# Kernel optimization log

Hardware: AMD Instinct MI355X
Metric: run time of the kernel (lower is better)

Reference implementation:

```python
import jax, jax.numpy as jnp
import numpy as np

N_NODES = 50000
N_EDGES = 20000
EDGE_SIZE = 32
IN_CH = 256
OUT_CH = 256


def setup_inputs() -> dict:
    key = jax.random.key(0)
    k1, k2, k3 = jax.random.split(key, 3)
    x = jax.random.normal(k1, (N_NODES, IN_CH), dtype=jnp.float32)
    hyperedges = jax.random.randint(k2, (N_EDGES, EDGE_SIZE), 0, N_NODES)
    weight = jax.random.normal(k3, (IN_CH, OUT_CH), dtype=jnp.float32)
    return {"x": x, "hyperedges": hyperedges, "weight": weight}


def reference(x, hyperedges, weight):
    # Gather node features per hyperedge and reduce ('sum' aggregation):
    # [E, K, C] -> [E, C]
    edge_sum = x[hyperedges].sum(axis=1)
    # Scatter-add each hyperedge's summed feature back to every member node.
    agg = jnp.zeros_like(x).at[hyperedges].add(edge_sum[:, None, :])
    # Dense projection + ReLU.
    return jax.nn.relu(agg @ weight)
```

## Files before the change

kernel.cpp:

```cpp
#include <hip/hip_runtime.h>
#include <hip/hip_bf16.h>
#include <hip/hip_fp16.h>

#define N_NODES 50000
#define N_EDGES 20000
#define EDGE_K  32
#define CH      256
#define N_INC   (N_EDGES * EDGE_K)
#define ELL_CAP 64
#define NSLICE  8
#define SCH     32
#define ZROW    N_EDGES

typedef __attribute__((ext_vector_type(4))) float f32x4;
typedef __attribute__((ext_vector_type(8))) _Float16 f16x8;

static __device__ __forceinline__ __half2 u2h2(unsigned int u) {
    __half2 h; __builtin_memcpy(&h, &u, 4); return h;
}
static __device__ __forceinline__ unsigned int h22u(__half2 h) {
    unsigned int u; __builtin_memcpy(&u, &h, 4); return u;
}
static __device__ __forceinline__ unsigned int pk2h(float a, float b) {
    return h22u(__halves2half2(__float2half_rn(a), __float2half_rn(b)));
}

#define FILL_GROUPS   8
#define NODES_PER_GRP (N_NODES / FILL_GROUPS)
#define FILL_WIN      2560
#define FILL_BLOCKS   ((N_INC / FILL_WIN) * FILL_GROUPS)
#define CONV_BLOCKS   (N_NODES * CH / 8 / 256)
__global__ void prep_kernel(const float* __restrict__ x, unsigned short* __restrict__ xb,
                            const float* __restrict__ w, unsigned short* __restrict__ wt,
                            const int* __restrict__ he, int* __restrict__ deg,
                            unsigned short* __restrict__ ell, unsigned short* __restrict__ yb) {
    int b = blockIdx.x;
    if (b < FILL_BLOCKS) {
        int g  = b % FILL_GROUPS;
        int wn = b / FILL_GROUPS;
        int lo = g * NODES_PER_GRP, hi = lo + NODES_PER_GRP;
        int base = wn * FILL_WIN;
#pragma unroll
        for (int it = 0; it < FILL_WIN / 256; ++it) {
            int i = base + it * 256 + threadIdx.x;
            int node = he[i];
            if (node >= lo && node < hi) {
                int slot = atomicAdd(&deg[node], 1);
                if (slot < ELL_CAP)
                    ell[(size_t)node * ELL_CAP + slot] = (unsigned short)(i >> 5);
            }
        }
    } else if (b < FILL_BLOCKS + CONV_BLOCKS) {
        int i = (b - FILL_BLOCKS) * 256 + threadIdx.x;
        int n = i >> 5, sub = i & 31;
        int g = sub >> 2, cp = (sub & 3) * 8;
        const float* src = x + (size_t)n * CH + sub * 8;
        f32x4 v0 = *reinterpret_cast<const f32x4*>(src);
        f32x4 v1 = *reinterpret_cast<const f32x4*>(src + 4);
        uint4 u;
        u.x = pk2h(v0.x, v0.y);
        u.y = pk2h(v0.z, v0.w);
        u.z = pk2h(v1.x, v1.y);
        u.w = pk2h(v1.z, v1.w);
        *reinterpret_cast<uint4*>(xb + ((size_t)g * N_NODES + n) * SCH + cp) = u;
    } else if (b < FILL_BLOCKS + CONV_BLOCKS + CH) {
        int n = b - FILL_BLOCKS - CONV_BLOCKS;
        int k = threadIdx.x;
        __half h = __float2half_rn(w[k * CH + n]);
        wt[n * CH + k] = *reinterpret_cast<unsigned short*>(&h);
    } else {
        int g = threadIdx.x >> 5, c = threadIdx.x & 31;
        yb[((size_t)g * (N_EDGES + 1) + ZROW) * SCH + c] = 0;
    }
}

#define GGRP          (N_EDGES / 16)
#define GATHER_BLOCKS (GGRP * NSLICE)
__global__ __launch_bounds__(256, 4) void gather_kernel(
        const unsigned short* __restrict__ xb, const int* __restrict__ he,
        unsigned short* __restrict__ es) {
    int gb  = blockIdx.x;
    int g   = gb & 7;
    int grp = gb >> 3;
    int w = threadIdx.x >> 6, lane = threadIdx.x & 63;
    int ebase = grp * 16 + w * 4;
    const int* hp = he + (size_t)ebase * EDGE_K;
    int s = lane & 15;
    int ep = lane >> 4, k = (lane >> 2) & 3, q = lane & 3;
    int mA = hp[ep * 32 + s];
    int mB = hp[ep * 32 + 16 + s];
    const unsigned short* xg = xb + (size_t)g * N_NODES * SCH;
    int hb = lane & 48;
    int e0 = __shfl(mA, hb + ((0 + k) & 15), 64);
    int e1 = __shfl(mA, hb + ((4 + k) & 15), 64);
    int e2 = __shfl(mA, hb + ((8 + k) & 15), 64);
    int e3 = __shfl(mA, hb + ((12 + k) & 15), 64);
    int e4 = __shfl(mB, hb + ((0 + k) & 15), 64);
    int e5 = __shfl(mB, hb + ((4 + k) & 15), 64);
    int e6 = __shfl(mB, hb + ((8 + k) & 15), 64);
    int e7 = __shfl(mB, hb + ((12 + k) & 15), 64);
    uint4 d0 = *reinterpret_cast<const uint4*>(xg + (size_t)e0 * SCH + q * 8);
    uint4 d1 = *reinterpret_cast<const uint4*>(xg + (size_t)e1 * SCH + q * 8);
    uint4 d2 = *reinterpret_cast<const uint4*>(xg + (size_t)e2 * SCH + q * 8);
    uint4 d3 = *reinterpret_cast<const uint4*>(xg + (size_t)e3 * SCH + q * 8);
    uint4 d4 = *reinterpret_cast<const uint4*>(xg + (size_t)e4 * SCH + q * 8);
    uint4 d5 = *reinterpret_cast<const uint4*>(xg + (size_t)e5 * SCH + q * 8);
    uint4 d6 = *reinterpret_cast<const uint4*>(xg + (size_t)e6 * SCH + q * 8);
    uint4 d7 = *reinterpret_cast<const uint4*>(xg + (size_t)e7 * SCH + q * 8);
    __builtin_amdgcn_sched_barrier(0);
    __half2 a0 = u2h2(0u), a1 = u2h2(0u), a2 = u2h2(0u), a3 = u2h2(0u);
    a0 = __hadd2(a0, u2h2(d0.x)); a1 = __hadd2(a1, u2h2(d0.y));
    a2 = __hadd2(a2, u2h2(d0.z)); a3 = __hadd2(a3, u2h2(d0.w));
    a0 = __hadd2(a0, u2h2(d1.x)); a1 = __hadd2(a1, u2h2(d1.y));
    a2 = __hadd2(a2, u2h2(d1.z)); a3 = __hadd2(a3, u2h2(d1.w));
    a0 = __hadd2(a0, u2h2(d2.x)); a1 = __hadd2(a1, u2h2(d2.y));
    a2 = __hadd2(a2, u2h2(d2.z)); a3 = __hadd2(a3, u2h2(d2.w));
    a0 = __hadd2(a0, u2h2(d3.x)); a1 = __hadd2(a1, u2h2(d3.y));
    a2 = __hadd2(a2, u2h2(d3.z)); a3 = __hadd2(a3, u2h2(d3.w));
    a0 = __hadd2(a0, u2h2(d4.x)); a1 = __hadd2(a1, u2h2(d4.y));
    a2 = __hadd2(a2, u2h2(d4.z)); a3 = __hadd2(a3, u2h2(d4.w));
    a0 = __hadd2(a0, u2h2(d5.x)); a1 = __hadd2(a1, u2h2(d5.y));
    a2 = __hadd2(a2, u2h2(d5.z)); a3 = __hadd2(a3, u2h2(d5.w));
    a0 = __hadd2(a0, u2h2(d6.x)); a1 = __hadd2(a1, u2h2(d6.y));
    a2 = __hadd2(a2, u2h2(d6.z)); a3 = __hadd2(a3, u2h2(d6.w));
    a0 = __hadd2(a0, u2h2(d7.x)); a1 = __hadd2(a1, u2h2(d7.y));
    a2 = __hadd2(a2, u2h2(d7.z)); a3 = __hadd2(a3, u2h2(d7.w));
    a0 = __hadd2(a0, u2h2(__shfl_xor(h22u(a0), 4, 64)));
    a1 = __hadd2(a1, u2h2(__shfl_xor(h22u(a1), 4, 64)));
    a2 = __hadd2(a2, u2h2(__shfl_xor(h22u(a2), 4, 64)));
    a3 = __hadd2(a3, u2h2(__shfl_xor(h22u(a3), 4, 64)));
    a0 = __hadd2(a0, u2h2(__shfl_xor(h22u(a0), 8, 64)));
    a1 = __hadd2(a1, u2h2(__shfl_xor(h22u(a1), 8, 64)));
    a2 = __hadd2(a2, u2h2(__shfl_xor(h22u(a2), 8, 64)));
    a3 = __hadd2(a3, u2h2(__shfl_xor(h22u(a3), 8, 64)));
    if ((lane & 12) == 0) {
        uint4 u;
        u.x = h22u(a0); u.y = h22u(a1); u.z = h22u(a2); u.w = h22u(a3);
        *reinterpret_cast<uint4*>(es + (size_t)(ebase + ep) * CH + g * SCH + q * 8) = u;
    }
}

__global__ __launch_bounds__(256) void gemm_kernel(const unsigned short* __restrict__ es,
                                                   const unsigned short* __restrict__ wt,
                                                   unsigned short* __restrict__ yb) {
    int wid  = threadIdx.x >> 6;
    int lane = threadIdx.x & 63;
    int m0   = blockIdx.x * 64 + wid * 16;
    if (m0 >= N_EDGES) return;
    int lr = lane & 15;
    int lg = lane >> 4;

    f32x4 acc[16] = {};
    const unsigned short* arow = es + (size_t)(m0 + lr) * CH + lg * 8;
#pragma unroll
    for (int kk = 0; kk < CH; kk += 32) {
        f16x8 a = *reinterpret_cast<const f16x8*>(arow + kk);
#pragma unroll
        for (int nt = 0; nt < 16; ++nt) {
            f16x8 bb = *reinterpret_cast<const f16x8*>(
                wt + (size_t)(nt * 16 + lr) * CH + kk + lg * 8);
            acc[nt] = __builtin_amdgcn_mfma_f32_16x16x32_f16(a, bb, acc[nt], 0, 0, 0);
        }
    }
#pragma unroll
    for (int nt = 0; nt < 16; ++nt) {
#pragma unroll
        for (int r = 0; r < 4; ++r) {
            int row = m0 + lg * 4 + r;
            __half h = __float2half_rn(acc[nt][r]);
            yb[((size_t)(nt >> 1) * (N_EDGES + 1) + row) * SCH + (nt & 1) * 16 + lr] =
                *reinterpret_cast<unsigned short*>(&h);
        }
    }
}

#define AP_NPB    16
#define AP_BLOCKS ((N_NODES / AP_NPB) * NSLICE)
__global__ __launch_bounds__(256, 4) void apply_kernel(
        const unsigned short* __restrict__ yb, const int* __restrict__ deg,
        const unsigned short* __restrict__ ell, float* __restrict__ out) {
    int b = blockIdx.x;
    int g = b & 7;
    int w = threadIdx.x >> 6, lane = threadIdx.x & 63;
    int np = lane >> 4, s = lane & 15, k = (lane >> 2) & 3, q = lane & 3;
    int node = (b >> 3) * AP_NPB + w * 4 + np;
    int d = deg[node];
    if (d > ELL_CAP) d = ELL_CAP;
    const unsigned short* er = ell + (size_t)node * ELL_CAP;
    int m0 = er[s], m1 = er[16 + s], m2 = er[32 + s], m3 = er[48 + s];
    int dmax = d;
    dmax = max(dmax, __shfl_xor(dmax, 16, 64));
    dmax = max(dmax, __shfl_xor(dmax, 32, 64));
    const unsigned short* yg = yb + (size_t)g * (N_EDGES + 1) * SCH;
    int hb = lane & 48;
    int e0 = __shfl(m0, hb + 0 + k, 64);  e0 = (0 + k  < d) ? e0 : ZROW;
    int e1 = __shfl(m0, hb + 4 + k, 64);  e1 = (4 + k  < d) ? e1 : ZROW;
    int e2 = __shfl(m0, hb + 8 + k, 64);  e2 = (8 + k  < d) ? e2 : ZROW;
    int e3 = __shfl(m0, hb + 12 + k, 64); e3 = (12 + k < d) ? e3 : ZROW;
    int e4 = __shfl(m1, hb + 0 + k, 64);  e4 = (16 + k < d) ? e4 : ZROW;
    int e5 = __shfl(m1, hb + 4 + k, 64);  e5 = (20 + k < d) ? e5 : ZROW;
    int e6 = __shfl(m1, hb + 8 + k, 64);  e6 = (24 + k < d) ? e6 : ZROW;
    int e7 = __shfl(m1, hb + 12 + k, 64); e7 = (28 + k < d) ? e7 : ZROW;
    uint4 d0 = *reinterpret_cast<const uint4*>(yg + (size_t)e0 * SCH + q * 8);
    uint4 d1 = *reinterpret_cast<const uint4*>(yg + (size_t)e1 * SCH + q * 8);
    uint4 d2 = *reinterpret_cast<const uint4*>(yg + (size_t)e2 * SCH + q * 8);
    uint4 d3 = *reinterpret_cast<const uint4*>(yg + (size_t)e3 * SCH + q * 8);
    uint4 d4 = *reinterpret_cast<const uint4*>(yg + (size_t)e4 * SCH + q * 8);
    uint4 d5 = *reinterpret_cast<const uint4*>(yg + (size_t)e5 * SCH + q * 8);
    uint4 d6 = *reinterpret_cast<const uint4*>(yg + (size_t)e6 * SCH + q * 8);
    uint4 d7 = *reinterpret_cast<const uint4*>(yg + (size_t)e7 * SCH + q * 8);
    __builtin_amdgcn_sched_barrier(0);
    __half2 a0 = u2h2(0u), a1 = u2h2(0u), a2 = u2h2(0u), a3 = u2h2(0u);
    a0 = __hadd2(a0, u2h2(d0.x)); a1 = __hadd2(a1, u2h2(d0.y));
    a2 = __hadd2(a2, u2h2(d0.z)); a3 = __hadd2(a3, u2h2(d0.w));
    a0 = __hadd2(a0, u2h2(d1.x)); a1 = __hadd2(a1, u2h2(d1.y));
    a2 = __hadd2(a2, u2h2(d1.z)); a3 = __hadd2(a3, u2h2(d1.w));
    a0 = __hadd2(a0, u2h2(d2.x)); a1 = __hadd2(a1, u2h2(d2.y));
    a2 = __hadd2(a2, u2h2(d2.z)); a3 = __hadd2(a3, u2h2(d2.w));
    a0 = __hadd2(a0, u2h2(d3.x)); a1 = __hadd2(a1, u2h2(d3.y));
    a2 = __hadd2(a2, u2h2(d3.z)); a3 = __hadd2(a3, u2h2(d3.w));
    a0 = __hadd2(a0, u2h2(d4.x)); a1 = __hadd2(a1, u2h2(d4.y));
    a2 = __hadd2(a2, u2h2(d4.z)); a3 = __hadd2(a3, u2h2(d4.w));
    a0 = __hadd2(a0, u2h2(d5.x)); a1 = __hadd2(a1, u2h2(d5.y));
    a2 = __hadd2(a2, u2h2(d5.z)); a3 = __hadd2(a3, u2h2(d5.w));
    a0 = __hadd2(a0, u2h2(d6.x)); a1 = __hadd2(a1, u2h2(d6.y));
    a2 = __hadd2(a2, u2h2(d6.z)); a3 = __hadd2(a3, u2h2(d6.w));
    a0 = __hadd2(a0, u2h2(d7.x)); a1 = __hadd2(a1, u2h2(d7.y));
    a2 = __hadd2(a2, u2h2(d7.z)); a3 = __hadd2(a3, u2h2(d7.w));
    if (dmax > 32) {
        int f0 = __shfl(m2, hb + 0 + k, 64);  f0 = (32 + k < d) ? f0 : ZROW;
        int f1 = __shfl(m2, hb + 4 + k, 64);  f1 = (36 + k < d) ? f1 : ZROW;
        int f2 = __shfl(m2, hb + 8 + k, 64);  f2 = (40 + k < d) ? f2 : ZROW;
        int f3 = __shfl(m2, hb + 12 + k, 64); f3 = (44 + k < d) ? f3 : ZROW;
        int f4 = __shfl(m3, hb + 0 + k, 64);  f4 = (48 + k < d) ? f4 : ZROW;
        int f5 = __shfl(m3, hb + 4 + k, 64);  f5 = (52 + k < d) ? f5 : ZROW;
        int f6 = __shfl(m3, hb + 8 + k, 64);  f6 = (56 + k < d) ? f6 : ZROW;
        int f7 = __shfl(m3, hb + 12 + k, 64); f7 = (60 + k < d) ? f7 : ZROW;
        uint4 c0 = *reinterpret_cast<const uint4*>(yg + (size_t)f0 * SCH + q * 8);
        uint4 c1 = *reinterpret_cast<const uint4*>(yg + (size_t)f1 * SCH + q * 8);
        uint4 c2 = *reinterpret_cast<const uint4*>(yg + (size_t)f2 * SCH + q * 8);
        uint4 c3 = *reinterpret_cast<const uint4*>(yg + (size_t)f3 * SCH + q * 8);
        uint4 c4 = *reinterpret_cast<const uint4*>(yg + (size_t)f4 * SCH + q * 8);
        uint4 c5 = *reinterpret_cast<const uint4*>(yg + (size_t)f5 * SCH + q * 8);
        uint4 c6 = *reinterpret_cast<const uint4*>(yg + (size_t)f6 * SCH + q * 8);
        uint4 c7 = *reinterpret_cast<const uint4*>(yg + (size_t)f7 * SCH + q * 8);
        a0 = __hadd2(a0, u2h2(c0.x)); a1 = __hadd2(a1, u2h2(c0.y));
        a2 = __hadd2(a2, u2h2(c0.z)); a3 = __hadd2(a3, u2h2(c0.w));
        a0 = __hadd2(a0, u2h2(c1.x)); a1 = __hadd2(a1, u2h2(c1.y));
        a2 = __hadd2(a2, u2h2(c1.z)); a3 = __hadd2(a3, u2h2(c1.w));
        a0 = __hadd2(a0, u2h2(c2.x)); a1 = __hadd2(a1, u2h2(c2.y));
        a2 = __hadd2(a2, u2h2(c2.z)); a3 = __hadd2(a3, u2h2(c2.w));
        a0 = __hadd2(a0, u2h2(c3.x)); a1 = __hadd2(a1, u2h2(c3.y));
        a2 = __hadd2(a2, u2h2(c3.z)); a3 = __hadd2(a3, u2h2(c3.w));
        a0 = __hadd2(a0, u2h2(c4.x)); a1 = __hadd2(a1, u2h2(c4.y));
        a2 = __hadd2(a2, u2h2(c4.z)); a3 = __hadd2(a3, u2h2(c4.w));
        a0 = __hadd2(a0, u2h2(c5.x)); a1 = __hadd2(a1, u2h2(c5.y));
        a2 = __hadd2(a2, u2h2(c5.z)); a3 = __hadd2(a3, u2h2(c5.w));
        a0 = __hadd2(a0, u2h2(c6.x)); a1 = __hadd2(a1, u2h2(c6.y));
        a2 = __hadd2(a2, u2h2(c6.z)); a3 = __hadd2(a3, u2h2(c6.w));
        a0 = __hadd2(a0, u2h2(c7.x)); a1 = __hadd2(a1, u2h2(c7.y));
        a2 = __hadd2(a2, u2h2(c7.z)); a3 = __hadd2(a3, u2h2(c7.w));
    }
    a0 = __hadd2(a0, u2h2(__shfl_xor(h22u(a0), 4, 64)));
    a1 = __hadd2(a1, u2h2(__shfl_xor(h22u(a1), 4, 64)));
    a2 = __hadd2(a2, u2h2(__shfl_xor(h22u(a2), 4, 64)));
    a3 = __hadd2(a3, u2h2(__shfl_xor(h22u(a3), 4, 64)));
    a0 = __hadd2(a0, u2h2(__shfl_xor(h22u(a0), 8, 64)));
    a1 = __hadd2(a1, u2h2(__shfl_xor(h22u(a1), 8, 64)));
    a2 = __hadd2(a2, u2h2(__shfl_xor(h22u(a2), 8, 64)));
    a3 = __hadd2(a3, u2h2(__shfl_xor(h22u(a3), 8, 64)));
    if ((lane & 12) == 0) {
        float2 f0 = __half22float2(a0);
        float2 f1 = __half22float2(a1);
        float2 f2 = __half22float2(a2);
        float2 f3 = __half22float2(a3);
        f32x4 r0, r1;
        r0.x = fmaxf(f0.x, 0.f); r0.y = fmaxf(f0.y, 0.f);
        r0.z = fmaxf(f1.x, 0.f); r0.w = fmaxf(f1.y, 0.f);
        r1.x = fmaxf(f2.x, 0.f); r1.y = fmaxf(f2.y, 0.f);
        r1.z = fmaxf(f3.x, 0.f); r1.w = fmaxf(f3.y, 0.f);
        float* dst = out + (size_t)node * CH + g * SCH + q * 8;
        *reinterpret_cast<f32x4*>(dst)     = r0;
        *reinterpret_cast<f32x4*>(dst + 4) = r1;
    }
}

extern "C" void kernel_launch(void* const* d_in, const int* in_sizes, int n_in,
                              void* d_out, int out_size, void* d_ws, size_t ws_size,
                              hipStream_t stream) {
    const float* x  = (const float*)d_in[0];
    const int*   he = (const int*)d_in[1];
    const float* w  = (const float*)d_in[2];
    float* out = (float*)d_out;

    char* ws = (char*)d_ws;
    unsigned short* wt  = (unsigned short*)ws;
    unsigned short* es  = (unsigned short*)(ws + 131072);
    unsigned short* yb  = (unsigned short*)(ws + 10371072);
    int* deg = (int*)(ws + 20611584);
    unsigned short* ell = (unsigned short*)(ws + 20811584);

    unsigned short* xb = (unsigned short*)d_out;

    hipMemsetAsync(deg, 0, (size_t)N_NODES * 4, stream);

    prep_kernel<<<FILL_BLOCKS + CONV_BLOCKS + CH + 1, 256, 0, stream>>>(
        x, xb, w, wt, he, deg, ell, yb);

    gather_kernel<<<GATHER_BLOCKS, 256, 0, stream>>>(xb, he, es);

    {
        int blocks = (N_EDGES + 63) / 64;
        gemm_kernel<<<blocks, 256, 0, stream>>>(es, wt, yb);
    }

    apply_kernel<<<AP_BLOCKS, 256, 0, stream>>>(yb, deg, ell, out);
}
```

Baseline: 146.5 us.

## Move ELL incidence fill from prep kernel into gather kernel launch

The hyperedge-to-node ELL fill (atomic degree counting and slot writes) moves out of the prep kernel into the gather kernel as extra leading blocks, so it overlaps with the feature gather rather than the fp16 conversion. The fill loop now loads all indices before issuing atomics to raise memory-level parallelism. It also removes the sched_barrier calls in gather and apply, and defers loading the upper ELL entries in apply until a node's degree exceeds 32. This shifts load balance between kernels. The gather launch grows with atomic-heavy blocks that may compete with gather blocks for bandwidth.

```diff
diff --git a/kernel.cpp b/kernel.cpp
--- a/kernel.cpp
+++ b/kernel.cpp
@@ -25,33 +25,13 @@
     return h22u(__halves2half2(__float2half_rn(a), __float2half_rn(b)));
 }
 
-#define FILL_GROUPS   8
-#define NODES_PER_GRP (N_NODES / FILL_GROUPS)
-#define FILL_WIN      2560
-#define FILL_BLOCKS   ((N_INC / FILL_WIN) * FILL_GROUPS)
-#define CONV_BLOCKS   (N_NODES * CH / 8 / 256)
+#define CONV_BLOCKS (N_NODES * CH / 8 / 256)
 __global__ void prep_kernel(const float* __restrict__ x, unsigned short* __restrict__ xb,
                             const float* __restrict__ w, unsigned short* __restrict__ wt,
-                            const int* __restrict__ he, int* __restrict__ deg,
-                            unsigned short* __restrict__ ell, unsigned short* __restrict__ yb) {
+                            unsigned short* __restrict__ yb) {
     int b = blockIdx.x;
-    if (b < FILL_BLOCKS) {
-        int g  = b % FILL_GROUPS;
-        int wn = b / FILL_GROUPS;
-        int lo = g * NODES_PER_GRP, hi = lo + NODES_PER_GRP;
-        int base = wn * FILL_WIN;
-#pragma unroll
-        for (int it = 0; it < FILL_WIN / 256; ++it) {
-            int i = base + it * 256 + threadIdx.x;
-            int node = he[i];
-            if (node >= lo && node < hi) {
-                int slot = atomicAdd(&deg[node], 1);
-                if (slot < ELL_CAP)
-                    ell[(size_t)node * ELL_CAP + slot] = (unsigned short)(i >> 5);
-            }
-        }
-    } else if (b < FILL_BLOCKS + CONV_BLOCKS) {
-        int i = (b - FILL_BLOCKS) * 256 + threadIdx.x;
+    if (b < CONV_BLOCKS) {
+        int i = b * 256 + threadIdx.x;
         int n = i >> 5, sub = i & 31;
         int g = sub >> 2, cp = (sub & 3) * 8;
         const float* src = x + (size_t)n * CH + sub * 8;
@@ -63,8 +43,8 @@
         u.z = pk2h(v1.x, v1.y);
         u.w = pk2h(v1.z, v1.w);
         *reinterpret_cast<uint4*>(xb + ((size_t)g * N_NODES + n) * SCH + cp) = u;
-    } else if (b < FILL_BLOCKS + CONV_BLOCKS + CH) {
-        int n = b - FILL_BLOCKS - CONV_BLOCKS;
+    } else if (b < CONV_BLOCKS + CH) {
+        int n = b - CONV_BLOCKS;
         int k = threadIdx.x;
         __half h = __float2half_rn(w[k * CH + n]);
         wt[n * CH + k] = *reinterpret_cast<unsigned short*>(&h);
@@ -74,12 +54,37 @@
     }
 }
 
-#define GGRP          (N_EDGES / 16)
-#define GATHER_BLOCKS (GGRP * NSLICE)
-__global__ __launch_bounds__(256, 4) void gather_kernel(
+#define FILL_GROUPS   8
+#define NODES_PER_GRP (N_NODES / FILL_GROUPS)
+#define FILL_WIN      2560
+#define FILL_BLOCKS   ((N_INC / FILL_WIN) * FILL_GROUPS)
+#define GATHER_BLOCKS ((N_EDGES / 16) * NSLICE)
+__global__ __launch_bounds__(256, 4) void gather_fill_kernel(
         const unsigned short* __restrict__ xb, const int* __restrict__ he,
-        unsigned short* __restrict__ es) {
-    int gb  = blockIdx.x;
+        unsigned short* __restrict__ es, int* __restrict__ deg,
+        unsigned short* __restrict__ ell) {
+    int b = blockIdx.x;
+    if (b < FILL_BLOCKS) {
+        int g  = b & 7;
+        int wn = b >> 3;
+        int lo = g * NODES_PER_GRP, hi = lo + NODES_PER_GRP;
+        int base = wn * FILL_WIN + threadIdx.x;
+        int idx[FILL_WIN / 256];
+#pragma unroll
+        for (int it = 0; it < FILL_WIN / 256; ++it) idx[it] = he[base + it * 256];
+#pragma unroll
+        for (int it = 0; it < FILL_WIN / 256; ++it) {
+            int node = idx[it];
+            if (node >= lo && node < hi) {
+                int slot = atomicAdd(&deg[node], 1);
+                if (slot < ELL_CAP)
+                    ell[(size_t)node * ELL_CAP + slot] =
+                        (unsigned short)((base + it * 256) >> 5);
+            }
+        }
+        return;
+    }
+    int gb  = b - FILL_BLOCKS;
     int g   = gb & 7;
     int grp = gb >> 3;
     int w = threadIdx.x >> 6, lane = threadIdx.x & 63;
@@ -107,7 +112,6 @@
     uint4 d5 = *reinterpret_cast<const uint4*>(xg + (size_t)e5 * SCH + q * 8);
     uint4 d6 = *reinterpret_cast<const uint4*>(xg + (size_t)e6 * SCH + q * 8);
     uint4 d7 = *reinterpret_cast<const uint4*>(xg + (size_t)e7 * SCH + q * 8);
-    __builtin_amdgcn_sched_barrier(0);
     __half2 a0 = u2h2(0u), a1 = u2h2(0u), a2 = u2h2(0u), a3 = u2h2(0u);
     a0 = __hadd2(a0, u2h2(d0.x)); a1 = __hadd2(a1, u2h2(d0.y));
     a2 = __hadd2(a2, u2h2(d0.z)); a3 = __hadd2(a3, u2h2(d0.w));
@@ -187,7 +191,7 @@
     int d = deg[node];
     if (d > ELL_CAP) d = ELL_CAP;
     const unsigned short* er = ell + (size_t)node * ELL_CAP;
-    int m0 = er[s], m1 = er[16 + s], m2 = er[32 + s], m3 = er[48 + s];
+    int m0 = er[s], m1 = er[16 + s];
     int dmax = d;
     dmax = max(dmax, __shfl_xor(dmax, 16, 64));
     dmax = max(dmax, __shfl_xor(dmax, 32, 64));
@@ -209,7 +213,6 @@
     uint4 d5 = *reinterpret_cast<const uint4*>(yg + (size_t)e5 * SCH + q * 8);
     uint4 d6 = *reinterpret_cast<const uint4*>(yg + (size_t)e6 * SCH + q * 8);
     uint4 d7 = *reinterpret_cast<const uint4*>(yg + (size_t)e7 * SCH + q * 8);
-    __builtin_amdgcn_sched_barrier(0);
     __half2 a0 = u2h2(0u), a1 = u2h2(0u), a2 = u2h2(0u), a3 = u2h2(0u);
     a0 = __hadd2(a0, u2h2(d0.x)); a1 = __hadd2(a1, u2h2(d0.y));
     a2 = __hadd2(a2, u2h2(d0.z)); a3 = __hadd2(a3, u2h2(d0.w));
@@ -228,6 +231,7 @@
     a0 = __hadd2(a0, u2h2(d7.x)); a1 = __hadd2(a1, u2h2(d7.y));
     a2 = __hadd2(a2, u2h2(d7.z)); a3 = __hadd2(a3, u2h2(d7.w));
     if (dmax > 32) {
+        int m2 = er[32 + s], m3 = er[48 + s];
         int f0 = __shfl(m2, hb + 0 + k, 64);  f0 = (32 + k < d) ? f0 : ZROW;
         int f1 = __shfl(m2, hb + 4 + k, 64);  f1 = (36 + k < d) ? f1 : ZROW;
         int f2 = __shfl(m2, hb + 8 + k, 64);  f2 = (40 + k < d) ? f2 : ZROW;
@@ -304,10 +308,9 @@
 
     hipMemsetAsync(deg, 0, (size_t)N_NODES * 4, stream);
 
-    prep_kernel<<<FILL_BLOCKS + CONV_BLOCKS + CH + 1, 256, 0, stream>>>(
-        x, xb, w, wt, he, deg, ell, yb);
-
-    gather_kernel<<<GATHER_BLOCKS, 256, 0, stream>>>(xb, he, es);
+    prep_kernel<<<CONV_BLOCKS + CH + 1, 256, 0, stream>>>(x, xb, w, wt, yb);
+
+    gather_fill_kernel<<<FILL_BLOCKS + GATHER_BLOCKS, 256, 0, stream>>>(xb, he, es, deg, ell);
 
     {
         int blocks = (N_EDGES + 63) / 64;
```

Result: no change. 146.3 us (-0.2%).
